# Performance work log

Measured on AMD Instinct MI355X. Metric: run time of the kernel, lower is better.

## Reference

```python
import jax, jax.numpy as jnp
import numpy as np

N = 10000
E = 160000
F_IN = 2000
HID = 128
NC = 5


def setup_inputs() -> dict:
    key = jax.random.key(0)
    ks = jax.random.split(key, 16)
    s = 0.05
    nrm = lambda k, shape: jax.random.normal(k, shape, jnp.float32) * s
    return {
        "x": jax.random.normal(ks[0], (N, F_IN), jnp.float32),
        "edge_index": jax.random.randint(ks[1], (2, E), 0, N),
        # GATConv 1: in=F_IN, out=HID, heads=6, concat=False
        "W_gat1": nrm(ks[2], (F_IN, 6 * HID)), "a_src1": nrm(ks[3], (6, HID)),
        "a_dst1": nrm(ks[4], (6, HID)), "b_gat1": jnp.zeros(HID, jnp.float32),
        # GCNConv 1
        "W_gcn1": nrm(ks[5], (HID, HID)), "b_gcn1": jnp.zeros(HID, jnp.float32),
        # GATConv 2: heads=4
        "W_gat2": nrm(ks[6], (HID, 4 * HID)), "a_src2": nrm(ks[7], (4, HID)),
        "a_dst2": nrm(ks[8], (4, HID)), "b_gat2": jnp.zeros(HID, jnp.float32),
        # GCNConv 2: out=HID//2
        "W_gcn2": nrm(ks[9], (HID, HID // 2)), "b_gcn2": jnp.zeros(HID // 2, jnp.float32),
        # skip projection / fusion
        "W_skip": nrm(ks[10], (F_IN, HID // 2)), "b_skip": jnp.zeros(HID // 2, jnp.float32),
        "W_fuse": nrm(ks[11], (HID + HID // 2, HID // 2)), "b_fuse": jnp.zeros(HID // 2, jnp.float32),
        # classifier MLP
        "W_c1": nrm(ks[12], (HID // 2, HID // 4)), "b_c1": jnp.zeros(HID // 4, jnp.float32),
        "W_c2": nrm(ks[13], (HID // 4, HID // 8)), "b_c2": jnp.zeros(HID // 8, jnp.float32),
        "W_c3": nrm(ks[14], (HID // 8, NC)), "b_c3": jnp.zeros(NC, jnp.float32),
        # LayerNorms
        "g1": jnp.ones(HID, jnp.float32), "be1": jnp.zeros(HID, jnp.float32),
        "g2": jnp.ones(HID, jnp.float32), "be2": jnp.zeros(HID, jnp.float32),
        "g3": jnp.ones(HID // 2, jnp.float32), "be3": jnp.zeros(HID // 2, jnp.float32),
    }


def layer_norm(x, g, b, eps=1e-5):
    mu = jnp.mean(x, axis=-1, keepdims=True)
    var = jnp.var(x, axis=-1, keepdims=True)
    return (x - mu) * jax.lax.rsqrt(var + eps) * g + b


def gat_conv(x, src, dst, W, a_src, a_dst, b, n):
    # PyG GATConv with concat=False (head-mean). Eval mode -> no attn dropout.
    H, C = a_src.shape
    h = (x @ W).reshape(-1, H, C)                      # [N,H,C]
    alpha = (h * a_src).sum(-1)[src] + (h * a_dst).sum(-1)[dst]  # [E,H]
    alpha = jax.nn.leaky_relu(alpha, 0.2)
    m = jax.ops.segment_max(alpha, dst, num_segments=n)
    e = jnp.exp(alpha - m[dst])
    w = e / jax.ops.segment_sum(e, dst, num_segments=n)[dst]     # segment softmax over incoming edges
    out = jax.ops.segment_sum(h[src] * w[:, :, None], dst, num_segments=n)  # [N,H,C]
    return out.mean(axis=1) + b


def gcn_conv(x, src, dst, W, b, n):
    deg = jax.ops.segment_sum(jnp.ones_like(dst, x.dtype), dst, num_segments=n)
    dinv = jnp.where(deg > 0, deg ** -0.5, 0.0)
    msg = (x @ W)[src] * (dinv[src] * dinv[dst])[:, None]
    return jax.ops.segment_sum(msg, dst, num_segments=n) + b


def reference(x, edge_index, W_gat1, a_src1, a_dst1, b_gat1, W_gcn1, b_gcn1,
              W_gat2, a_src2, a_dst2, b_gat2, W_gcn2, b_gcn2,
              W_skip, b_skip, W_fuse, b_fuse, W_c1, b_c1, W_c2, b_c2, W_c3, b_c3,
              g1, be1, g2, be2, g3, be3):
    n = x.shape[0]
    loop = jnp.arange(n, dtype=edge_index.dtype)
    src = jnp.concatenate([edge_index[0], loop])  # add_self_loops
    dst = jnp.concatenate([edge_index[1], loop])

    x1_gat = jax.nn.relu(layer_norm(gat_conv(x, src, dst, W_gat1, a_src1, a_dst1, b_gat1, n), g1, be1))
    x1_gcn = jax.nn.relu(gcn_conv(x1_gat, src, dst, W_gcn1, b_gcn1, n))
    x2_gat = jax.nn.relu(layer_norm(gat_conv(x1_gcn, src, dst, W_gat2, a_src2, a_dst2, b_gat2, n), g2, be2))
    x2_gcn = jax.nn.relu(gcn_conv(x2_gat, src, dst, W_gcn2, b_gcn2, n))

    skip = jax.nn.relu(x @ W_skip + b_skip)
    fused = jax.nn.relu(jnp.concatenate([x1_gcn, x2_gcn], axis=1) @ W_fuse + b_fuse)
    final = layer_norm(fused + skip, g3, be3)

    h = jax.nn.relu(final @ W_c1 + b_c1)
    h = jax.nn.relu(h @ W_c2 + b_c2)
    return h @ W_c3 + b_c3
```

## Files before the change

kernel.cpp:

```cpp
#include <hip/hip_runtime.h>
#include <cstdint>
#include <cstddef>

#define NN 10000
#define NE 160000
#define ET (NE + NN)
#define FIN 2000
#define MPAD 10112
#define KPAD 2048
#define NPAD 896

typedef __bf16 bf16x8 __attribute__((ext_vector_type(8)));
typedef __bf16 bf16x4 __attribute__((ext_vector_type(4)));
typedef float  f32x4  __attribute__((ext_vector_type(4)));

#define GLL(src, dst) __builtin_amdgcn_global_load_lds( \
    (const __attribute__((address_space(1))) void*)(src), \
    (__attribute__((address_space(3))) void*)(dst), 16, 0, 0)

__device__ __forceinline__ void edge_sd(const int* ei, int e, int& s, int& d) {
    if (e < NE) { s = ei[e]; d = ei[NE + e]; }
    else        { s = e - NE; d = e - NE; }
}

__global__ void scan_kernel(const int* deg, int* rowstart, float* dinv) {
    __shared__ int partial[256];
    const int T = 256;
    int chunk = (NN + T - 1) / T;
    int t = threadIdx.x;
    int begin = t * chunk;
    int end = begin + chunk; if (end > NN) end = NN;
    int s = 0;
    for (int i = begin; i < end && i >= begin; i++) s += deg[i];
    partial[t] = s;
    __syncthreads();
    if (t == 0) {
        int run = 0;
        for (int i = 0; i < T; i++) { int v = partial[i]; partial[i] = run; run += v; }
    }
    __syncthreads();
    int run = partial[t];
    for (int i = begin; i < end && i >= begin; i++) {
        rowstart[i] = run; run += deg[i];
        int dg = deg[i];
        dinv[i] = dg > 0 ? rsqrtf((float)dg) : 0.f;
    }
    if (end == NN && begin <= NN) rowstart[NN] = run;
}

__global__ void scatter_kernel(const int* ei, const int* rowstart, int* cursor,
                               int* csr_src) {
    int e = blockIdx.x * blockDim.x + threadIdx.x;
    if (e >= ET) return;
    int s, d; edge_sd(ei, e, s, d);
    int pos = atomicAdd(&cursor[d], 1);
    csr_src[rowstart[d] + pos] = s;
}

#define NBX (158 * 32)
#define NW1 (NPAD * KPAD / 8)
#define NWT (NW1 + 512 * 128 / 8)
#define NWT2 (NWT + 2048 + 1024)
#define WBLK ((NWT2 + 255) / 256)
#define EB 665
__global__ void conv_kernel(const float* __restrict__ x, __bf16* __restrict__ xb,
                            const float* __restrict__ Wg, const float* __restrict__ Ws,
                            const float* __restrict__ W2,
                            const float* __restrict__ Wg1, const float* __restrict__ Wg2,
                            __bf16* __restrict__ wt, __bf16* __restrict__ w2t,
                            __bf16* __restrict__ wgcn1s, __bf16* __restrict__ wgcn2s,
                            const int* __restrict__ ei, int* __restrict__ deg) {
    __shared__ __bf16 slab[4096];
    int bid = blockIdx.x;
    int tid = threadIdx.x;
    if (bid < NBX) {
        int rt = bid >> 5, ks = bid & 31;
        int r = tid >> 2;
        int row = rt * 64 + r;
        int c0 = (tid & 3) * 16;
        int kbase = ks * 64;
#pragma unroll
        for (int j = 0; j < 4; j++) {
            int kl = c0 + j * 4;
            int k = kbase + kl;
            bf16x4 o;
            if (row < NN && k + 3 < FIN) {
                float4 v = *(const float4*)(x + (size_t)row * FIN + k);
                o[0] = (__bf16)v.x; o[1] = (__bf16)v.y;
                o[2] = (__bf16)v.z; o[3] = (__bf16)v.w;
            } else {
                o[0] = o[1] = o[2] = o[3] = (__bf16)0.f;
            }
            int p = kl >> 3, off = kl & 7;
            *(bf16x4*)(slab + (p * 64 + r) * 8 + off) = o;
        }
        __syncthreads();
        size_t base = (size_t)(rt * 32 + ks) * 512;
#pragma unroll
        for (int i = 0; i < 2; i++) {
            int c = i * 256 + tid;
            *(bf16x8*)(xb + (base + c) * 8) = *(const bf16x8*)(slab + c * 8);
        }
    } else if (bid < NBX + WBLK) {
        int g = (bid - NBX) * 256 + tid;
        if (g < NW1) {
            int r = g & 127, p = (g >> 7) & 7, ks = (g >> 10) & 31, ct = g >> 15;
            int n = ct * 128 + r;
            int k0 = ks * 64 + p * 8;
            bf16x8 o;
#pragma unroll
            for (int j = 0; j < 8; j++) {
                int k = k0 + j;
                float v = 0.f;
                if (k < FIN) {
                    if (n < 768)      v = Wg[(size_t)k * 768 + n];
                    else if (n < 832) v = Ws[(size_t)k * 64 + (n - 768)];
                }
                o[j] = (__bf16)v;
            }
            *(bf16x8*)(wt + (size_t)g * 8) = o;
        } else if (g < NWT) {
            int g2 = g - NW1;
            int c = g2 & 2047;
            int ct = g2 >> 11;
            int p = c >> 7, r = c & 127;
            int n = ct * 128 + r;
            int k0 = p * 8;
            bf16x8 o;
#pragma unroll
            for (int j = 0; j < 8; j++)
                o[j] = (__bf16)W2[(size_t)(k0 + j) * 512 + n];
            *(bf16x8*)(w2t + (size_t)g2 * 8) = o;
        } else if (g < NWT + 2048) {
            int g3 = g - NWT;
            int p = g3 >> 7, r = g3 & 127;
            bf16x8 o;
#pragma unroll
            for (int j = 0; j < 8; j++)
                o[j] = (__bf16)Wg1[(size_t)(p * 8 + j) * 128 + r];
            *(bf16x8*)(wgcn1s + (size_t)g3 * 8) = o;
        } else if (g < NWT2) {
            int g4 = g - NWT - 2048;
            int p = g4 >> 6, r = g4 & 63;
            bf16x8 o;
#pragma unroll
            for (int j = 0; j < 8; j++)
                o[j] = (__bf16)Wg2[(size_t)(p * 8 + j) * 64 + r];
            *(bf16x8*)(wgcn2s + (size_t)g4 * 8) = o;
        }
    } else {
        int e = (bid - NBX - WBLK) * 256 + tid;
        if (e < ET) {
            int s, d; edge_sd(ei, e, s, d);
            atomicAdd(&deg[d], 1);
        }
    }
}

__global__ __launch_bounds__(256)
void mfma_gemm1_kernel(const __bf16* __restrict__ xb, const __bf16* __restrict__ wt,
                       const float* __restrict__ a_src1, const float* __restrict__ a_dst1,
                       __bf16* __restrict__ h1b, float* __restrict__ skippre,
                       float* __restrict__ asrc, float* __restrict__ adst) {
    __shared__ __bf16 As[8192];
    __shared__ __bf16 Bs[8192];
    __shared__ float sA[128], sD[128];
    __shared__ float asd[256];
    int b = blockIdx.x;
    int xcd = b & 7, j = b >> 3;
    int jq = j / 7;
    int rt = xcd + 8 * jq;
    int ct = j - 7 * jq;
    if (rt >= MPAD / 128) return;
    const int bi = rt * 128;
    const int bn = ct * 128;

    const int tid = threadIdx.x;
    const int lane = tid & 63;
    const int w = tid >> 6;
    const int wm = w >> 1, wn = w & 1;
    const int q = lane >> 4, m16 = lane & 15;

    if (tid < 128) { sA[tid] = 0.f; sD[tid] = 0.f; }
    if (ct < 6) {
        if (tid < 128) asd[tid] = a_src1[ct * 128 + tid];
        else           asd[tid] = a_dst1[ct * 128 + (tid - 128)];
    }

    f32x4 acc[4][4] = {};

    for (int ks = 0; ks < KPAD / 64; ks++) {
        const size_t slabA = ((size_t)(rt * 2) * 32 + ks) * 512;
        const size_t slabB = ((size_t)ct * 32 + ks) * 1024;
#pragma unroll
        for (int i = 0; i < 4; i++) {
            int seg = i * 4 + w;
            int p = seg >> 1, h = seg & 1;
            GLL(xb + (slabA + (size_t)h * 16384 + p * 64 + lane) * 8,
                As + seg * 512);
        }
#pragma unroll
        for (int i = 0; i < 4; i++) {
            int seg = i * 4 + w;
            GLL(wt + (slabB + seg * 64 + lane) * 8, Bs + seg * 512);
        }
        __syncthreads();

#pragma unroll
        for (int kk = 0; kk < 2; kk++) {
            const int pb = kk * 4 + q;
            bf16x8 bfr[4];
#pragma unroll
            for (int nt = 0; nt < 4; nt++)
                bfr[nt] = *(const bf16x8*)(Bs + (pb * 128 + wn * 64 + nt * 16 + m16) * 8);
#pragma unroll
            for (int mt = 0; mt < 4; mt++) {
                bf16x8 af = *(const bf16x8*)(As + (pb * 128 + wm * 64 + mt * 16 + m16) * 8);
#pragma unroll
                for (int nt = 0; nt < 4; nt++)
                    acc[mt][nt] = __builtin_amdgcn_mfma_f32_16x16x32_bf16(af, bfr[nt], acc[mt][nt], 0, 0, 0);
            }
        }
        __syncthreads();
    }

#pragma unroll
    for (int mt = 0; mt < 4; mt++) {
#pragma unroll
        for (int r = 0; r < 4; r++) {
            int rowl = wm * 64 + mt * 16 + q * 4 + r;
            int row = bi + rowl;
            float ps = 0.f, pd = 0.f;
#pragma unroll
            for (int nt = 0; nt < 4; nt++) {
                int coll = wn * 64 + nt * 16 + m16;
                int col = bn + coll;
                float v = acc[mt][nt][r];
                if (ct < 6) { ps += v * asd[coll]; pd += v * asd[128 + coll]; }
                if (row < NN) {
                    if (col < 768)      h1b[(size_t)row * 768 + col] = (__bf16)v;
                    else if (col < 832) skippre[(size_t)row * 64 + (col - 768)] = v;
                }
            }
            if (ct < 6) {
#pragma unroll
                for (int off = 1; off < 16; off <<= 1) {
                    ps += __shfl_xor(ps, off);
                    pd += __shfl_xor(pd, off);
                }
                if (m16 == 0) { atomicAdd(&sA[rowl], ps); atomicAdd(&sD[rowl], pd); }
            }
        }
    }
    if (ct < 6) {
        __syncthreads();
        if (tid < 128) {
            int row = bi + tid;
            if (row < NN) { asrc[row * 6 + ct] = sA[tid]; adst[row * 6 + ct] = sD[tid]; }
        }
    }
}

__global__ __launch_bounds__(256)
void mfma_gemm2_kernel(const __bf16* __restrict__ A, const __bf16* __restrict__ B,
                       const float* __restrict__ a_src2, const float* __restrict__ a_dst2,
                       __bf16* __restrict__ h2b,
                       float* __restrict__ asrc, float* __restrict__ adst) {
    __shared__ __bf16 As[4096];
    __shared__ __bf16 Bs[8192];
    __shared__ float sA[64], sD[64];
    __shared__ float asd[256];
    const int rt = blockIdx.y, ct = blockIdx.x;
    const int bi = rt * 64, bn = ct * 128;
    const int tid = threadIdx.x, lane = tid & 63, w = tid >> 6;
    const int wm = w >> 1, wn = w & 1;
    const int q = lane >> 4, m16 = lane & 15;

    if (tid < 64) { sA[tid] = 0.f; sD[tid] = 0.f; }
    if (tid < 128) asd[tid] = a_src2[ct * 128 + tid];
    else           asd[tid] = a_dst2[ct * 128 + (tid - 128)];

    f32x4 acc[2][4] = {};

    for (int ks = 0; ks < 2; ks++) {
        const size_t slabA = (size_t)rt * 1024 + ks * 512;
        const size_t slabB = (size_t)ct * 2048 + ks * 1024;
#pragma unroll
        for (int i = 0; i < 2; i++) {
            int seg = i * 4 + w;
            GLL(A + (slabA + seg * 64 + lane) * 8, As + seg * 512);
        }
#pragma unroll
        for (int i = 0; i < 4; i++) {
            int seg = i * 4 + w;
            GLL(B + (slabB + seg * 64 + lane) * 8, Bs + seg * 512);
        }
        __syncthreads();

#pragma unroll
        for (int kk = 0; kk < 2; kk++) {
            const int pb = kk * 4 + q;
            bf16x8 af[2], bfr[4];
#pragma unroll
            for (int mt = 0; mt < 2; mt++)
                af[mt] = *(const bf16x8*)(As + (pb * 64 + wm * 32 + mt * 16 + m16) * 8);
#pragma unroll
            for (int nt = 0; nt < 4; nt++)
                bfr[nt] = *(const bf16x8*)(Bs + (pb * 128 + wn * 64 + nt * 16 + m16) * 8);
#pragma unroll
            for (int mt = 0; mt < 2; mt++)
#pragma unroll
                for (int nt = 0; nt < 4; nt++)
                    acc[mt][nt] = __builtin_amdgcn_mfma_f32_16x16x32_bf16(af[mt], bfr[nt], acc[mt][nt], 0, 0, 0);
        }
        __syncthreads();
    }

#pragma unroll
    for (int mt = 0; mt < 2; mt++) {
#pragma unroll
        for (int r = 0; r < 4; r++) {
            int rowl = wm * 32 + mt * 16 + q * 4 + r;
            int row = bi + rowl;
            float ps = 0.f, pd = 0.f;
#pragma unroll
            for (int nt = 0; nt < 4; nt++) {
                int coll = wn * 64 + nt * 16 + m16;
                float v = acc[mt][nt][r];
                ps += v * asd[coll]; pd += v * asd[128 + coll];
                if (row < NN) h2b[(size_t)row * 512 + bn + coll] = (__bf16)v;
            }
#pragma unroll
            for (int off = 1; off < 16; off <<= 1) {
                ps += __shfl_xor(ps, off);
                pd += __shfl_xor(pd, off);
            }
            if (m16 == 0) { atomicAdd(&sA[rowl], ps); atomicAdd(&sD[rowl], pd); }
        }
    }
    __syncthreads();
    if (tid < 64) {
        int row = bi + tid;
        if (row < NN) { asrc[row * 4 + ct] = sA[tid]; adst[row * 4 + ct] = sD[tid]; }
    }
}

template<int NT>
__global__ __launch_bounds__(256)
void mfma_gcn_kernel(const __bf16* __restrict__ A, const __bf16* __restrict__ B,
                     __bf16* __restrict__ Cb) {
    __shared__ __bf16 As[4096];
    __shared__ __bf16 Bs[NT * 64];
    const int rt = blockIdx.x;
    const int bi = rt * 64;
    const int tid = threadIdx.x, lane = tid & 63, w = tid >> 6;
    const int q = lane >> 4, m16 = lane & 15;
    constexpr int MT = (NT == 128) ? 2 : 1;
    constexpr int MSPAN = (NT == 128) ? 32 : 16;
    const int wm = (NT == 128) ? (w >> 1) : w;
    const int wn = (NT == 128) ? (w & 1) : 0;

    f32x4 acc[MT][4] = {};

    for (int ks = 0; ks < 2; ks++) {
        const size_t slabA = (size_t)rt * 1024 + ks * 512;
        const size_t slabB = (size_t)ks * (NT * 8);
#pragma unroll
        for (int i = 0; i < 2; i++) {
            int seg = i * 4 + w;
            GLL(A + (slabA + seg * 64 + lane) * 8, As + seg * 512);
        }
#pragma unroll
        for (int i = 0; i < NT / 32; i++) {
            int seg = i * 4 + w;
            GLL(B + (slabB + (size_t)seg * 64 + lane) * 8, Bs + seg * 512);
        }
        __syncthreads();

#pragma unroll
        for (int kk = 0; kk < 2; kk++) {
            const int pb = kk * 4 + q;
            bf16x8 af[MT], bfr[4];
#pragma unroll
            for (int mt = 0; mt < MT; mt++)
                af[mt] = *(const bf16x8*)(As + (pb * 64 + wm * MSPAN + mt * 16 + m16) * 8);
#pragma unroll
            for (int nt = 0; nt < 4; nt++)
                bfr[nt] = *(const bf16x8*)(Bs + (pb * NT + wn * 64 + nt * 16 + m16) * 8);
#pragma unroll
            for (int mt = 0; mt < MT; mt++)
#pragma unroll
                for (int nt = 0; nt < 4; nt++)
                    acc[mt][nt] = __builtin_amdgcn_mfma_f32_16x16x32_bf16(af[mt], bfr[nt], acc[mt][nt], 0, 0, 0);
        }
        __syncthreads();
    }

#pragma unroll
    for (int mt = 0; mt < MT; mt++) {
#pragma unroll
        for (int r = 0; r < 4; r++) {
            int row = bi + wm * MSPAN + mt * 16 + q * 4 + r;
            if (row >= NN) continue;
#pragma unroll
            for (int nt = 0; nt < 4; nt++) {
                int col = wn * 64 + nt * 16 + m16;
                Cb[(size_t)row * NT + col] = (__bf16)acc[mt][nt][r];
            }
        }
    }
}

template<int H>
__global__ void gat_agg_kernel(const __bf16* __restrict__ hb,
                               const float* __restrict__ asrc,
                               const float* __restrict__ adst,
                               const int* __restrict__ rowstart,
                               const int* __restrict__ csr_src,
                               const float* __restrict__ bias,
                               const float* __restrict__ gamma,
                               const float* __restrict__ beta,
                               __bf16* __restrict__ outs) {
    constexpr int CH = H * 128;
    constexpr int CAP = 128;
    int n = blockIdx.x;
    int t = threadIdx.x;
    int w = t >> 6, l = t & 63;
    __shared__ float invden[H];
    __shared__ float denw[4][H];
    __shared__ int   srcs[CAP];
    __shared__ float evs[CAP * H];
    __shared__ float sm[4 * CH];
    __shared__ float red[8];

    int s0 = rowstart[n];
    int deg = rowstart[n + 1] - s0;
    float adst_n = (l < H) ? adst[n * H + l] : 0.f;

    float dloc = 0.f;
    for (int idx = w; idx < deg; idx += 4) {
        int src = csr_src[s0 + idx];
        if (idx < CAP && l == 0) srcs[idx] = src;
        if (l < H) {
            float al = asrc[src * H + l] + adst_n;
            al = al >= 0.f ? al : 0.2f * al;
            float ev = __expf(al);
            dloc += ev;
            if (idx < CAP) evs[idx * H + l] = ev;
        }
    }
    if (l < H) denw[w][l] = dloc;
    __syncthreads();
    if (t < H) invden[t] = 1.f / (denw[0][t] + denw[1][t] + denw[2][t] + denw[3][t]);
    __syncthreads();

    constexpr int NA = (H == 6) ? 12 : 8;
    float acc[NA] = {};
    const int h0 = l >> 4;
    const int h1i = 4 + (l >> 5);
    int degc = deg < CAP ? deg : CAP;
    int idx = w;
    for (; idx + 4 < degc; idx += 8) {
        int src0 = srcs[idx], src1 = srcs[idx + 4];
        float w00 = evs[idx * H + h0];
        float w10 = evs[(idx + 4) * H + h0];
        const __bf16* hp0 = hb + (size_t)src0 * CH;
        const __bf16* hp1 = hb + (size_t)src1 * CH;
        bf16x8 g00 = *(const bf16x8*)(hp0 + l * 8);
        bf16x8 g10 = *(const bf16x8*)(hp1 + l * 8);
#pragma unroll
        for (int jj = 0; jj < 8; jj++)
            acc[jj] += (float)g00[jj] * w00 + (float)g10[jj] * w10;
        if (H == 6) {
            float w01 = evs[idx * H + h1i];
            float w11 = evs[(idx + 4) * H + h1i];
            bf16x4 g01 = *(const bf16x4*)(hp0 + 512 + l * 4);
            bf16x4 g11 = *(const bf16x4*)(hp1 + 512 + l * 4);
#pragma unroll
            for (int jj = 0; jj < 4; jj++)
                acc[8 + jj] += (float)g01[jj] * w01 + (float)g11[jj] * w11;
        }
    }
    if (idx < degc) {
        int src = srcs[idx];
        float w0 = evs[idx * H + h0];
        const __bf16* hp = hb + (size_t)src * CH;
        bf16x8 hv = *(const bf16x8*)(hp + l * 8);
#pragma unroll
        for (int jj = 0; jj < 8; jj++) acc[jj] += (float)hv[jj] * w0;
        if (H == 6) {
            float w1 = evs[idx * H + h1i];
            bf16x4 hv1 = *(const bf16x4*)(hp + 512 + l * 4);
#pragma unroll
            for (int jj = 0; jj < 4; jj++) acc[8 + jj] += (float)hv1[jj] * w1;
        }
    }
    for (int i2 = CAP + w; i2 < deg; i2 += 4) {
        int src = csr_src[s0 + i2];
        float ev = 0.f;
        if (l < H) {
            float al = asrc[src * H + l] + adst_n;
            al = al >= 0.f ? al : 0.2f * al;
            ev = __expf(al);
        }
        const __bf16* hp = hb + (size_t)src * CH;
        float wgt = __shfl(ev, h0);
        bf16x8 hv = *(const bf16x8*)(hp + l * 8);
#pragma unroll
        for (int jj = 0; jj < 8; jj++) acc[jj] += (float)hv[jj] * wgt;
        if (H == 6) {
            float wg1 = __shfl(ev, h1i);
            bf16x4 hv1 = *(const bf16x4*)(hp + 512 + l * 4);
#pragma unroll
            for (int jj = 0; jj < 4; jj++) acc[8 + jj] += (float)hv1[jj] * wg1;
        }
    }

    *(f32x4*)(sm + w * CH + l * 8)     = *(f32x4*)(acc);
    *(f32x4*)(sm + w * CH + l * 8 + 4) = *(f32x4*)(acc + 4);
    if (H == 6)
        *(f32x4*)(sm + w * CH + 512 + l * 4) = *(f32x4*)(acc + 8);
    __syncthreads();

    float v = 0.f;
    if (t < 128) {
#pragma unroll
        for (int hh = 0; hh < H; hh++) {
            float hsum = 0.f;
#pragma unroll
            for (int ww = 0; ww < 4; ww++) hsum += sm[ww * CH + hh * 128 + t];
            v += hsum * invden[hh];
        }
        v = v * (1.f / H) + bias[t];
    }
    float sv = (t < 128) ? v : 0.f;
    float sq = (t < 128) ? v * v : 0.f;
#pragma unroll
    for (int off = 32; off; off >>= 1) {
        sv += __shfl_down(sv, off);
        sq += __shfl_down(sq, off);
    }
    if ((t & 63) == 0) { red[w * 2] = sv; red[w * 2 + 1] = sq; }
    __syncthreads();
    float tot = red[0] + red[2] + red[4] + red[6];
    float tsq = red[1] + red[3] + red[5] + red[7];
    float mu = tot * (1.f / 128.f);
    float var = tsq * (1.f / 128.f) - mu * mu;
    float r = rsqrtf(var + 1e-5f);
    if (t < 128) {
        float o = fmaxf((v - mu) * r * gamma[t] + beta[t], 0.f);
        int rt2 = n >> 6, rr = n & 63, pp = t >> 3, off2 = t & 7;
        outs[((size_t)(rt2 * 16 + pp) * 64 + rr) * 8 + off2] = (__bf16)o;
    }
}

__global__ void gcn_agg_kernel(const __bf16* __restrict__ y, int C,
                               const float* __restrict__ dinv,
                               const int* __restrict__ rowstart,
                               const int* __restrict__ csr_src,
                               const float* __restrict__ bias,
                               float* __restrict__ out, int ldo, int coloff,
                               __bf16* __restrict__ bout) {
    int n = blockIdx.x;
    int t = threadIdx.x;
    float acc = 0.f;
    int s0 = rowstart[n], s1 = rowstart[n + 1];
    for (int s = s0; s < s1; s++) {
        int src = csr_src[s];
        acc += (float)y[(size_t)src * C + t] * dinv[src];
    }
    float v = fmaxf(acc * dinv[n] + bias[t], 0.f);
    out[(size_t)n * ldo + coloff + t] = v;
    if (bout) {
        int rt = n >> 6, r = n & 63, p = t >> 3, off = t & 7;
        bout[((size_t)(rt * 16 + p) * 64 + r) * 8 + off] = (__bf16)v;
    }
}

__global__ __launch_bounds__(256)
void fuse_final_kernel(const float* __restrict__ cat,
                       const float* __restrict__ skippre,
                       const float* __restrict__ Wf, const float* __restrict__ bfz,
                       const float* __restrict__ b_skip,
                       const float* __restrict__ g3, const float* __restrict__ be3,
                       const float* __restrict__ Wc1, const float* __restrict__ bc1,
                       const float* __restrict__ Wc2, const float* __restrict__ bc2,
                       const float* __restrict__ Wc3, const float* __restrict__ bc3,
                       float* __restrict__ out) {
    __shared__ float WfS[192 * 64];
    __shared__ float catS[4][196];
    __shared__ float fS[4][64], h1S[4][32], h2S[4][16];
    int tid = threadIdx.x;
    int w = tid >> 6, l = tid & 63;
#pragma unroll
    for (int i = 0; i < 12; i++) {
        int idx = (i * 256 + tid) * 4;
        *(f32x4*)(WfS + idx) = *(const f32x4*)(Wf + idx);
    }
    int n = blockIdx.x * 4 + w;
    bool act = n < NN;
    float sk = 0.f;
    if (act) {
        catS[w][l]       = cat[(size_t)n * 192 + l];
        catS[w][64 + l]  = cat[(size_t)n * 192 + 64 + l];
        catS[w][128 + l] = cat[(size_t)n * 192 + 128 + l];
        sk = fmaxf(skippre[(size_t)n * 64 + l] + b_skip[l], 0.f);
    }
    __syncthreads();

    float fu = bfz[l];
#pragma unroll 4
    for (int k = 0; k < 192; k++)
        fu += catS[w][k] * WfS[k * 64 + l];
    float v = fmaxf(fu, 0.f) + sk;

    float sv = v, sq = v * v;
#pragma unroll
    for (int off = 32; off; off >>= 1) {
        sv += __shfl_xor(sv, off);
        sq += __shfl_xor(sq, off);
    }
    float mu = sv * (1.f / 64.f);
    float var = sq * (1.f / 64.f) - mu * mu;
    float r = rsqrtf(var + 1e-5f);
    fS[w][l] = (v - mu) * r * g3[l] + be3[l];
    __syncthreads();
    if (l < 32) {
        float a = bc1[l];
        for (int i = 0; i < 64; i++) a += fS[w][i] * Wc1[i * 32 + l];
        h1S[w][l] = fmaxf(a, 0.f);
    }
    __syncthreads();
    if (l < 16) {
        float a = bc2[l];
        for (int i = 0; i < 32; i++) a += h1S[w][i] * Wc2[i * 16 + l];
        h2S[w][l] = fmaxf(a, 0.f);
    }
    __syncthreads();
    if (l < 5 && act) {
        float a = bc3[l];
        for (int i = 0; i < 16; i++) a += h2S[w][i] * Wc3[i * 5 + l];
        out[(size_t)n * 5 + l] = a;
    }
}

extern "C" void kernel_launch(void* const* d_in, const int* in_sizes, int n_in,
                              void* d_out, int out_size, void* d_ws, size_t ws_size,
                              hipStream_t stream) {
    const float* x      = (const float*)d_in[0];
    const int*   ei     = (const int*)d_in[1];
    const float* W_gat1 = (const float*)d_in[2];
    const float* a_src1 = (const float*)d_in[3];
    const float* a_dst1 = (const float*)d_in[4];
    const float* b_gat1 = (const float*)d_in[5];
    const float* W_gcn1 = (const float*)d_in[6];
    const float* b_gcn1 = (const float*)d_in[7];
    const float* W_gat2 = (const float*)d_in[8];
    const float* a_src2 = (const float*)d_in[9];
    const float* a_dst2 = (const float*)d_in[10];
    const float* b_gat2 = (const float*)d_in[11];
    const float* W_gcn2 = (const float*)d_in[12];
    const float* b_gcn2 = (const float*)d_in[13];
    const float* W_skip = (const float*)d_in[14];
    const float* b_skip = (const float*)d_in[15];
    const float* W_fuse = (const float*)d_in[16];
    const float* b_fuse = (const float*)d_in[17];
    const float* W_c1   = (const float*)d_in[18];
    const float* b_c1   = (const float*)d_in[19];
    const float* W_c2   = (const float*)d_in[20];
    const float* b_c2   = (const float*)d_in[21];
    const float* W_c3   = (const float*)d_in[22];
    const float* b_c3   = (const float*)d_in[23];
    const float* g1     = (const float*)d_in[24];
    const float* be1    = (const float*)d_in[25];
    const float* g2     = (const float*)d_in[26];
    const float* be2    = (const float*)d_in[27];
    const float* g3     = (const float*)d_in[28];
    const float* be3    = (const float*)d_in[29];
    float* out = (float*)d_out;

    char* p = (char*)d_ws;
    auto alloc = [&](size_t bytes) {
        char* r = p; p += (bytes + 255) & ~(size_t)255; return r;
    };
    __bf16* xb      = (__bf16*)alloc((size_t)MPAD * KPAD * 2);
    __bf16* wt      = (__bf16*)alloc((size_t)NPAD * KPAD * 2);
    __bf16* w2t     = (__bf16*)alloc((size_t)512 * 128 * 2);
    __bf16* wgcn1s  = (__bf16*)alloc((size_t)128 * 128 * 2);
    __bf16* wgcn2s  = (__bf16*)alloc((size_t)64 * 128 * 2);
    __bf16* h1b     = (__bf16*)alloc((size_t)NN * 768 * 2);
    __bf16* h2b     = (__bf16*)alloc((size_t)NN * 512 * 2);
    __bf16* ybufb   = (__bf16*)alloc((size_t)NN * 128 * 2);
    __bf16* x1gatb  = (__bf16*)alloc((size_t)3 * MPAD * 128 * 2);
    __bf16* x1gcnb  = x1gatb + (size_t)MPAD * 128;
    __bf16* x2gatb  = x1gcnb + (size_t)MPAD * 128;
    float* asrc     = (float*)alloc((size_t)NN * 6 * 4);
    float* adst     = (float*)alloc((size_t)NN * 6 * 4);
    int*   deg      = (int*)  alloc((size_t)2 * NN * 4);
    int*   cursor   = deg + NN;
    float* dinv     = (float*)alloc((size_t)NN * 4);
    int*   rowst    = (int*)  alloc((size_t)(NN + 1) * 4);
    int*   csrc     = (int*)  alloc((size_t)ET * 4);
    float* cat      = (float*)alloc((size_t)NN * 192 * 4);
    float* skippre  = (float*)alloc((size_t)NN * 64 * 4);

    hipMemsetAsync(deg, 0, (size_t)2 * NN * 4, stream);
    hipMemsetAsync(x1gatb, 0, (size_t)3 * MPAD * 128 * 2, stream);

    conv_kernel<<<NBX + WBLK + EB, 256, 0, stream>>>(
        x, xb, W_gat1, W_skip, W_gat2, W_gcn1, W_gcn2,
        wt, w2t, wgcn1s, wgcn2s, ei, deg);

    scan_kernel   <<<1, 256, 0, stream>>>(deg, rowst, dinv);
    scatter_kernel<<<EB, 256, 0, stream>>>(ei, rowst, cursor, csrc);

    mfma_gemm1_kernel<<<560, 256, 0, stream>>>(xb, wt, a_src1, a_dst1,
                                               h1b, skippre, asrc, adst);

    gat_agg_kernel<6><<<NN, 256, 0, stream>>>(h1b, asrc, adst, rowst, csrc,
                                              b_gat1, g1, be1, x1gatb);
    mfma_gcn_kernel<128><<<MPAD / 64, 256, 0, stream>>>(x1gatb, wgcn1s, ybufb);
    gcn_agg_kernel<<<NN, 128, 0, stream>>>(ybufb, 128, dinv, rowst, csrc,
                                           b_gcn1, cat, 192, 0, x1gcnb);
    mfma_gemm2_kernel<<<dim3(4, MPAD / 64), 256, 0, stream>>>(
        x1gcnb, w2t, a_src2, a_dst2, h2b, asrc, adst);
    gat_agg_kernel<4><<<NN, 256, 0, stream>>>(h2b, asrc, adst, rowst, csrc,
                                              b_gat2, g2, be2, x2gatb);
    mfma_gcn_kernel<64><<<MPAD / 64, 256, 0, stream>>>(x2gatb, wgcn2s, ybufb);
    gcn_agg_kernel<<<NN, 64, 0, stream>>>(ybufb, 64, dinv, rowst, csrc,
                                          b_gcn2, cat, 192, 128, nullptr);
    fuse_final_kernel<<<(NN + 3) / 4, 256, 0, stream>>>(
        cat, skippre, W_fuse, b_fuse, b_skip, g3, be3,
        W_c1, b_c1, W_c2, b_c2, W_c3, b_c3, out);
}
```

Baseline: 491.2 us.

## Use 8 waves in GEMM1 and parallelize GAT attention-score pass across edges

GEMM1 now launches 512 threads per block, with each of 8 waves computing a 32x64 sub-tile instead of 4 waves computing 64x64. This halves per-thread accumulators and load work, trading fewer registers per thread for more waves per block to improve latency hiding. The GAT aggregation's first pass now spreads 32 edges across the block at once (8 threads per edge, one per head) instead of one edge per wave with only H lanes active. Per-head denominators are then reduced from 32 partial sums.

```diff
diff --git a/kernel.cpp b/kernel.cpp
--- a/kernel.cpp
+++ b/kernel.cpp
@@ -157,7 +157,7 @@
     }
 }
 
-__global__ __launch_bounds__(256)
+__global__ __launch_bounds__(512)
 void mfma_gemm1_kernel(const __bf16* __restrict__ xb, const __bf16* __restrict__ wt,
                        const float* __restrict__ a_src1, const float* __restrict__ a_dst1,
                        __bf16* __restrict__ h1b, float* __restrict__ skippre,
@@ -178,30 +178,31 @@
     const int tid = threadIdx.x;
     const int lane = tid & 63;
     const int w = tid >> 6;
-    const int wm = w >> 1, wn = w & 1;
+    const int wm = w >> 1;
+    const int wn = w & 1;
     const int q = lane >> 4, m16 = lane & 15;
 
     if (tid < 128) { sA[tid] = 0.f; sD[tid] = 0.f; }
     if (ct < 6) {
-        if (tid < 128) asd[tid] = a_src1[ct * 128 + tid];
-        else           asd[tid] = a_dst1[ct * 128 + (tid - 128)];
-    }
-
-    f32x4 acc[4][4] = {};
+        if (tid < 128)      asd[tid] = a_src1[ct * 128 + tid];
+        else if (tid < 256) asd[tid] = a_dst1[ct * 128 + (tid - 128)];
+    }
+
+    f32x4 acc[2][4] = {};
 
     for (int ks = 0; ks < KPAD / 64; ks++) {
         const size_t slabA = ((size_t)(rt * 2) * 32 + ks) * 512;
         const size_t slabB = ((size_t)ct * 32 + ks) * 1024;
 #pragma unroll
-        for (int i = 0; i < 4; i++) {
-            int seg = i * 4 + w;
+        for (int i = 0; i < 2; i++) {
+            int seg = i * 8 + w;
             int p = seg >> 1, h = seg & 1;
             GLL(xb + (slabA + (size_t)h * 16384 + p * 64 + lane) * 8,
                 As + seg * 512);
         }
 #pragma unroll
-        for (int i = 0; i < 4; i++) {
-            int seg = i * 4 + w;
+        for (int i = 0; i < 2; i++) {
+            int seg = i * 8 + w;
             GLL(wt + (slabB + seg * 64 + lane) * 8, Bs + seg * 512);
         }
         __syncthreads();
@@ -209,26 +210,27 @@
 #pragma unroll
         for (int kk = 0; kk < 2; kk++) {
             const int pb = kk * 4 + q;
-            bf16x8 bfr[4];
+            bf16x8 af[2], bfr[4];
+#pragma unroll
+            for (int mt = 0; mt < 2; mt++)
+                af[mt] = *(const bf16x8*)(As + (pb * 128 + wm * 32 + mt * 16 + m16) * 8);
 #pragma unroll
             for (int nt = 0; nt < 4; nt++)
                 bfr[nt] = *(const bf16x8*)(Bs + (pb * 128 + wn * 64 + nt * 16 + m16) * 8);
 #pragma unroll
-            for (int mt = 0; mt < 4; mt++) {
-                bf16x8 af = *(const bf16x8*)(As + (pb * 128 + wm * 64 + mt * 16 + m16) * 8);
+            for (int mt = 0; mt < 2; mt++)
 #pragma unroll
                 for (int nt = 0; nt < 4; nt++)
-                    acc[mt][nt] = __builtin_amdgcn_mfma_f32_16x16x32_bf16(af, bfr[nt], acc[mt][nt], 0, 0, 0);
-            }
+                    acc[mt][nt] = __builtin_amdgcn_mfma_f32_16x16x32_bf16(af[mt], bfr[nt], acc[mt][nt], 0, 0, 0);
         }
         __syncthreads();
     }
 
 #pragma unroll
-    for (int mt = 0; mt < 4; mt++) {
+    for (int mt = 0; mt < 2; mt++) {
 #pragma unroll
         for (int r = 0; r < 4; r++) {
-            int rowl = wm * 64 + mt * 16 + q * 4 + r;
+            int rowl = wm * 32 + mt * 16 + q * 4 + r;
             int row = bi + rowl;
             float ps = 0.f, pd = 0.f;
 #pragma unroll
@@ -427,7 +429,7 @@
     int t = threadIdx.x;
     int w = t >> 6, l = t & 63;
     __shared__ float invden[H];
-    __shared__ float denw[4][H];
+    __shared__ float denp[256];
     __shared__ int   srcs[CAP];
     __shared__ float evs[CAP * H];
     __shared__ float sm[4 * CH];
@@ -437,21 +439,32 @@
     int deg = rowstart[n + 1] - s0;
     float adst_n = (l < H) ? adst[n * H + l] : 0.f;
 
+    const int eh = t >> 3;
+    const int hh1 = t & 7;
+    float adst_h = (hh1 < H) ? adst[n * H + hh1] : 0.f;
     float dloc = 0.f;
-    for (int idx = w; idx < deg; idx += 4) {
-        int src = csr_src[s0 + idx];
-        if (idx < CAP && l == 0) srcs[idx] = src;
-        if (l < H) {
-            float al = asrc[src * H + l] + adst_n;
-            al = al >= 0.f ? al : 0.2f * al;
-            float ev = __expf(al);
-            dloc += ev;
-            if (idx < CAP) evs[idx * H + l] = ev;
-        }
-    }
-    if (l < H) denw[w][l] = dloc;
-    __syncthreads();
-    if (t < H) invden[t] = 1.f / (denw[0][t] + denw[1][t] + denw[2][t] + denw[3][t]);
+    for (int base = 0; base < deg; base += 32) {
+        int idx = base + eh;
+        if (idx < deg) {
+            int src = csr_src[s0 + idx];
+            if (hh1 == 0 && idx < CAP) srcs[idx] = src;
+            if (hh1 < H) {
+                float al = asrc[src * H + hh1] + adst_h;
+                al = al >= 0.f ? al : 0.2f * al;
+                float ev = __expf(al);
+                dloc += ev;
+                if (idx < CAP) evs[idx * H + hh1] = ev;
+            }
+        }
+    }
+    denp[t] = dloc;
+    __syncthreads();
+    if (t < H) {
+        float s = 0.f;
+#pragma unroll
+        for (int g = 0; g < 32; g++) s += denp[g * 8 + t];
+        invden[t] = 1.f / s;
+    }
     __syncthreads();
 
     constexpr int NA = (H == 6) ? 12 : 8;
@@ -714,7 +727,7 @@
     scan_kernel   <<<1, 256, 0, stream>>>(deg, rowst, dinv);
     scatter_kernel<<<EB, 256, 0, stream>>>(ei, rowst, cursor, csrc);
 
-    mfma_gemm1_kernel<<<560, 256, 0, stream>>>(xb, wt, a_src1, a_dst1,
+    mfma_gemm1_kernel<<<560, 512, 0, stream>>>(xb, wt, a_src1, a_dst1,
                                                h1b, skippre, asrc, adst);
 
     gat_agg_kernel<6><<<NN, 256, 0, stream>>>(h1b, asrc, adst, rowst, csrc,
```

After: 441.1 us. 1.11x faster.
